# Kernel tuning notes

Hardware: AMD Instinct MI355X
Metric: run time of the kernel (lower is better)

## Reference

```python
import jax, jax.numpy as jnp
import numpy as np

N_NODES = 20000
N_EDGES = 240000
NUM_SPECIES = 4
NUM_BASIS = 16
MAX_RADIUS = 3.15
SQRT_NN = float(np.sqrt(12.0))  # num_neighbors normalization


def _cg121():
    # Clebsch-Gordan for 1e x 2e -> 1e in the real l=2 basis used below:
    # [xy, yz, (3z^2-1), zx, x^2-y^2] (component-normalized). Built from the
    # symmetric traceless matrix pairing M(a) @ v, normalized to unit Frobenius norm.
    s5, s15 = np.sqrt(5.0), np.sqrt(15.0)
    C = np.zeros((3, 5, 3))
    for A in range(5):
        a = np.zeros(5); a[A] = 1.0
        M = np.zeros((3, 3))
        M[0, 1] = M[1, 0] = a[0] * s15 / 2
        M[1, 2] = M[2, 1] = a[1] * s15 / 2
        M[0, 2] = M[2, 0] = a[3] * s15 / 2
        M[0, 0] = -a[2] * s5 / 2 + a[4] * s15 / 2
        M[1, 1] = -a[2] * s5 / 2 - a[4] * s15 / 2
        M[2, 2] = a[2] * s5
        C[:, A, :] = M
    C /= np.linalg.norm(C)
    return jnp.asarray(C, dtype=jnp.float32)

CG121 = _cg121()


def silu(v):
    return v * jax.nn.sigmoid(v)


def lin0(h, W):  # equivariant linear on scalars: [N,u] x [u,v]
    return h @ W / np.sqrt(W.shape[0])


def lin1(h, W):  # equivariant linear on vectors: [N,u,3] x [u,v]
    return jnp.einsum('nuk,uv->nvk', h, W) / np.sqrt(W.shape[0])


def radial_mlp(hb, W1, W2):  # FullyConnectedNet([16,64,nw], silu), normalized weights
    h = silu(hb @ W1 / np.sqrt(W1.shape[0]))
    return h @ W2 / np.sqrt(W2.shape[0])


def radial_basis(r):
    # soft_one_hot_linspace(..., basis='smooth_finite', cutoff=True) * sqrt(NUM_BASIS)
    values = np.linspace(0.0, MAX_RADIUS, NUM_BASIS + 2, dtype=np.float32)[1:-1]
    step = float(values[1] - values[0])
    d = (r[:, None] - values) / step
    def sus(t):
        safe = jnp.where(t > 0, t, 1.0)
        return jnp.where(t > 0, jnp.exp(-1.0 / safe), 0.0)
    y = 1.14136 * float(np.exp(2.0)) * sus(1.0 + d) * sus(1.0 - d)
    return y * np.sqrt(float(NUM_BASIS))


def sph_harm(edge_vec):
    # normalize=True, normalization='component' real spherical harmonics, l=0,1,2
    r = jnp.linalg.norm(edge_vec, axis=1)
    u = edge_vec / r[:, None]
    ux, uy, uz = u[:, 0], u[:, 1], u[:, 2]
    sh1 = np.sqrt(3.0) * u
    sh2 = jnp.stack([np.sqrt(15.0) * ux * uy,
                     np.sqrt(15.0) * uy * uz,
                     np.sqrt(5.0) / 2 * (3 * uz * uz - 1.0),
                     np.sqrt(15.0) * uz * ux,
                     np.sqrt(15.0) / 2 * (ux * ux - uy * uy)], axis=1)
    return r, sh1, sh2


def _forward(x, edge_index, edge_vec, emb,
             L1_lin1_0, L1_W1, L1_W2, L1_lin2_0, L1_lin2_1, L1_sc_0,
             L2_lin1_0, L2_lin1_1, L2_W1, L2_W2, L2_lin2_0, L2_lin2_1, L2_sc_0, L2_sc_1,
             LO_lin1_0, LO_lin1_1, LO_W1, LO_W2, LO_lin2_0, LO_sc_0):
    src, dst = edge_index[0], edge_index[1]
    N = x.shape[0]
    h0 = emb[x]                                   # [N,64] node embedding
    r, sh1, sh2 = sph_harm(edge_vec)
    hb = radial_basis(r)                          # [E,16]

    # ---- interaction 1: 64x0e -> (144x0e + 16x1e) -> gate -> 128x0e + 16x1e
    sc0 = lin0(h0, L1_sc_0)                       # self-connection [N,144]
    x0 = lin0(h0, L1_lin1_0)[src]                 # [E,64]
    w = radial_mlp(hb, L1_W1, L1_W2)              # [E,128] TP weights (uvu)
    m0 = x0 * w[:, :64]                           # 0e x 0e -> 0e
    m1 = (x0 * w[:, 64:128])[:, :, None] * sh1[:, None, :]  # 0e x 1e -> 1e
    a0 = jax.ops.segment_sum(m0, dst, num_segments=N) / SQRT_NN
    a1 = jax.ops.segment_sum(m1, dst, num_segments=N) / SQRT_NN
    g0 = lin0(a0, L1_lin2_0) + sc0                # [N,144]
    g1 = lin1(a1, L1_lin2_1)                      # [N,16,3]
    h0 = silu(g0[:, :128])                        # gated scalars
    h1 = jax.nn.sigmoid(g0[:, 128:])[:, :, None] * g1  # gate 16x1e

    # ---- interaction 2: 128x0e+16x1e -> (144x0e + 176x1e mid) -> gate
    sc0 = lin0(h0, L2_sc_0)                       # [N,144]
    sc1 = lin1(h1, L2_sc_1)                       # [N,16,3]
    x0 = lin0(h0, L2_lin1_0)[src]                 # [E,128]
    x1 = lin1(h1, L2_lin1_1)[src]                 # [E,16,3]
    w = radial_mlp(hb, L2_W1, L2_W2)              # [E,320]
    m0a = x0 * w[:, :128]                                            # 0x0->0
    m0b = jnp.einsum('euk,ek->eu', x1, sh1) / np.sqrt(3.0) * w[:, 272:288]  # 1x1->0
    m1a = (x0 * w[:, 128:256])[:, :, None] * sh1[:, None, :]         # 0x1->1
    m1b = x1 * w[:, 256:272][:, :, None]                             # 1x0->1
    m1c = jnp.cross(x1, sh1[:, None, :]) / np.sqrt(6.0) * w[:, 288:304][:, :, None]  # 1x1->1
    m1d = jnp.einsum('eui,eA,iAk->euk', x1, sh2, CG121) * w[:, 304:320][:, :, None]  # 1x2->1
    mid0 = jnp.concatenate([m0a, m0b], axis=1)    # [E,144]
    mid1 = jnp.concatenate([m1a, m1b, m1c, m1d], axis=1)  # [E,176,3]
    a0 = jax.ops.segment_sum(mid0, dst, num_segments=N) / SQRT_NN
    a1 = jax.ops.segment_sum(mid1, dst, num_segments=N) / SQRT_NN
    g0 = lin0(a0, L2_lin2_0) + sc0
    g1 = lin1(a1, L2_lin2_1) + sc1
    h0 = silu(g0[:, :128])
    h1 = jax.nn.sigmoid(g0[:, 128:])[:, :, None] * g1

    # ---- output interaction: -> 4x0e
    sc0 = lin0(h0, LO_sc_0)                       # [N,4]
    x0 = lin0(h0, LO_lin1_0)[src]
    x1 = lin1(h1, LO_lin1_1)[src]
    w = radial_mlp(hb, LO_W1, LO_W2)              # [E,144]
    m0a = x0 * w[:, :128]
    m0b = jnp.einsum('euk,ek->eu', x1, sh1) / np.sqrt(3.0) * w[:, 128:144]
    a0 = jax.ops.segment_sum(jnp.concatenate([m0a, m0b], axis=1), dst, num_segments=N) / SQRT_NN
    return lin0(a0, LO_lin2_0) + sc0              # [N,4]


def setup_inputs() -> dict:
    key = jax.random.key(0)
    ks = jax.random.split(key, 32)
    f = lambda i, shape: jax.random.normal(ks[i], shape, dtype=jnp.float32)
    return {
        'x': jax.random.randint(ks[0], (N_NODES,), 0, NUM_SPECIES),
        'edge_index': jax.random.randint(ks[1], (2, N_EDGES), 0, N_NODES),
        'edge_vec': jax.random.normal(ks[2], (N_EDGES, 3), dtype=jnp.float32),
        'emb': f(3, (NUM_SPECIES, 64)),
        'L1_lin1_0': f(4, (64, 64)),
        'L1_W1': f(5, (16, 64)), 'L1_W2': f(6, (64, 128)),
        'L1_lin2_0': f(7, (64, 144)), 'L1_lin2_1': f(8, (64, 16)),
        'L1_sc_0': f(9, (64, 144)),
        'L2_lin1_0': f(10, (128, 128)), 'L2_lin1_1': f(11, (16, 16)),
        'L2_W1': f(12, (16, 64)), 'L2_W2': f(13, (64, 320)),
        'L2_lin2_0': f(14, (144, 144)), 'L2_lin2_1': f(15, (176, 16)),
        'L2_sc_0': f(16, (128, 144)), 'L2_sc_1': f(17, (16, 16)),
        'LO_lin1_0': f(18, (128, 128)), 'LO_lin1_1': f(19, (16, 16)),
        'LO_W1': f(20, (16, 64)), 'LO_W2': f(21, (64, 144)),
        'LO_lin2_0': f(22, (144, 4)), 'LO_sc_0': f(23, (128, 4)),
    }


def reference(x, edge_index, edge_vec, emb,
              L1_lin1_0, L1_W1, L1_W2, L1_lin2_0, L1_lin2_1, L1_sc_0,
              L2_lin1_0, L2_lin1_1, L2_W1, L2_W2, L2_lin2_0, L2_lin2_1, L2_sc_0, L2_sc_1,
              LO_lin1_0, LO_lin1_1, LO_W1, LO_W2, LO_lin2_0, LO_sc_0):
    return _forward(x, edge_index, edge_vec, emb,
                    L1_lin1_0, L1_W1, L1_W2, L1_lin2_0, L1_lin2_1, L1_sc_0,
                    L2_lin1_0, L2_lin1_1, L2_W1, L2_W2, L2_lin2_0, L2_lin2_1, L2_sc_0, L2_sc_1,
                    LO_lin1_0, LO_lin1_1, LO_W1, LO_W2, LO_lin2_0, LO_sc_0)
```

## Files before the change

kernel.cpp:

```cpp
#include <hip/hip_runtime.h>
#include <math.h>

#define N_NODES 20000
#define N_EDGES 240000

typedef _Float16 half2_t __attribute__((ext_vector_type(2)));
typedef _Float16 f16x8   __attribute__((ext_vector_type(8)));
typedef float    f32x4v  __attribute__((ext_vector_type(4)));

__device__ __forceinline__ float siluf(float v){ return v * (1.0f/(1.0f+__expf(-v))); }
__device__ __forceinline__ float sigmf(float v){ return 1.0f/(1.0f+__expf(-v)); }

__global__ void k_count(const int* __restrict__ ei, int* __restrict__ cnt){
  int e = blockIdx.x*blockDim.x + threadIdx.x;
  if (e < N_EDGES) atomicAdd(&cnt[ei[N_EDGES + e]], 1);
}

__global__ void k_scan(const int* __restrict__ cnt, int* __restrict__ off, int* __restrict__ pos){
  __shared__ int part[1024];
  int t = threadIdx.x;
  int c[20]; int s = 0;
  #pragma unroll
  for (int j=0;j<20;j++){
    int idx = t*20 + j;
    int v = (idx < N_NODES) ? cnt[idx] : 0;
    c[j] = s; s += v;
  }
  part[t] = s;
  __syncthreads();
  for (int d=1; d<1024; d<<=1){
    int add = (t>=d) ? part[t-d] : 0;
    __syncthreads();
    part[t] += add;
    __syncthreads();
  }
  int excl = part[t] - s;
  #pragma unroll
  for (int j=0;j<20;j++){
    int idx = t*20 + j;
    if (idx < N_NODES){ off[idx] = excl + c[j]; pos[idx] = excl + c[j]; }
  }
  if (t == 1023) off[N_NODES] = part[1023];
}

__global__ void k_scatter(const int* __restrict__ ei, int* __restrict__ pos,
                          int* __restrict__ perm, int* __restrict__ srcs){
  int e = blockIdx.x*blockDim.x + threadIdx.x;
  if (e >= N_EDGES) return;
  int d = ei[N_EDGES + e];
  int p = atomicAdd(&pos[d], 1);
  perm[e] = p;
  srcs[p] = ei[e];
}

__global__ void k_geom(const float* __restrict__ ev, const int* __restrict__ perm,
                       float* __restrict__ eg){
  int e = blockIdx.x*blockDim.x + threadIdx.x;
  if (e >= N_EDGES) return;
  float x = ev[3*e+0], y = ev[3*e+1], z = ev[3*e+2];
  float r = sqrtf(x*x + y*y + z*z);
  float inv = 1.0f / fmaxf(r, 1e-12f);
  float ux = x*inv, uy = y*inv, uz = z*inv;
  float* o = eg + (size_t)perm[e]*24;
  o[0] = 1.7320508f*ux; o[1] = 1.7320508f*uy; o[2] = 1.7320508f*uz;
  o[3] = 3.8729833f*ux*uy;
  o[4] = 3.8729833f*uy*uz;
  o[5] = 1.1180340f*(3.0f*uz*uz - 1.0f);
  o[6] = 3.8729833f*uz*ux;
  o[7] = 1.9364917f*(ux*ux - uy*uy);
  const float invstep = 17.0f/3.15f;
  float t = r*invstep;
  #pragma unroll
  for (int i=0;i<16;i++){
    float d = t - (float)(i+1);
    float a = 1.0f + d, b = 1.0f - d;
    float v = 0.0f;
    if (a > 0.0f && b > 0.0f) v = 33.734292f*__expf(-1.0f/a - 1.0f/b);
    o[8+i] = v;
  }
}

__global__ void k_node_l1(const int* __restrict__ xs, const float* __restrict__ emb,
                          const float* __restrict__ Wlin, const float* __restrict__ Wsc,
                          float* __restrict__ X0, float* __restrict__ SC0){
  __shared__ float hs[4][64];
  int n0 = blockIdx.x*4;
  int t  = threadIdx.x;
  {
    int j = t>>6, k = t&63;
    hs[j][k] = emb[xs[n0+j]*64 + k];
  }
  __syncthreads();
  if (t < 64){
    float acc[4] = {};
    for (int k=0;k<64;k++){
      float wv = Wlin[k*64 + t];
      #pragma unroll
      for (int j=0;j<4;j++) acc[j] += hs[j][k]*wv;
    }
    #pragma unroll
    for (int j=0;j<4;j++) X0[(size_t)(n0+j)*64 + t] = acc[j]*0.125f;
  } else if (t < 208){
    int o = t - 64;
    float acc[4] = {};
    for (int k=0;k<64;k++){
      float wv = Wsc[k*144 + o];
      #pragma unroll
      for (int j=0;j<4;j++) acc[j] += hs[j][k]*wv;
    }
    #pragma unroll
    for (int j=0;j<4;j++) SC0[(size_t)(n0+j)*144 + o] = acc[j]*0.125f;
  }
}

__global__ __launch_bounds__(256) void k_hidden(
    const float* __restrict__ EG, const float* __restrict__ W1,
    _Float16* __restrict__ H){
  __shared__ float w1s[16*64];
  int tid = threadIdx.x;
  for (int i=tid;i<16*64;i+=256) w1s[i] = W1[i]*0.25f;
  __syncthreads();
  int lane = tid & 63, wib = tid >> 6;
  int gw = blockIdx.x*4 + wib, nw = gridDim.x*4;
  for (int e = gw; e < N_EDGES; e += nw){
    const float* g8 = EG + (size_t)e*24 + 8;
    float a0 = 0.0f, a1 = 0.0f;
    #pragma unroll
    for (int b=0;b<8;b++){
      a0 = fmaf(g8[b],   w1s[b*64 + lane],     a0);
      a1 = fmaf(g8[8+b], w1s[(8+b)*64 + lane], a1);
    }
    H[(size_t)e*64 + lane] = (_Float16)siluf(a0 + a1);
  }
}

template<int MODE>
__device__ __forceinline__ float colscale(int c){
  if constexpr (MODE == 1){
    if (c >= 272 && c < 288) return 0.57735027f;
    if (c >= 288 && c < 304) return 0.40824829f;
    return 1.0f;
  } else if constexpr (MODE == 2){
    return (c >= 128) ? 0.57735027f : 1.0f;
  }
  return 1.0f;
}

template<int NT, int MODE>
__global__ __launch_bounds__(256) void k_ww_mfma(
    int e0c, int e1c, const _Float16* __restrict__ H,
    const float* __restrict__ W2, _Float16* __restrict__ WW){
  constexpr int NCOL = NT*16;
  constexpr int NTW  = (NT + 3) / 4;
  int tid = threadIdx.x;
  int lane = tid & 63, wib = tid >> 6;
  int row = lane & 15, quad = lane >> 4;
  const float fold = 0.125f*0.28867513f;
  f16x8 B0[NTW], B1[NTW];
  #pragma unroll
  for (int t2=0; t2<NTW; t2++){
    int ct = wib*NTW + t2;
    int c  = ct*16 + row;
    bool valid = (ct < NT);
    float fs = valid ? fold*colscale<MODE>(c) : 0.0f;
    int ci = valid ? c : 0;
    #pragma unroll
    for (int j=0;j<8;j++){
      B0[t2][j] = (_Float16)(W2[(quad*8+j)*NCOL + ci]*fs);
      B1[t2][j] = (_Float16)(W2[(32+quad*8+j)*NCOL + ci]*fs);
    }
  }
  int ntiles = (e1c - e0c) >> 4;
  for (int t = blockIdx.x; t < ntiles; t += gridDim.x){
    int eb = e0c + t*16;
    const _Float16* hp = H + (size_t)(eb + row)*64 + quad*8;
    f16x8 A0 = *(const f16x8*)hp;
    f16x8 A1 = *(const f16x8*)(hp + 32);
    #pragma unroll
    for (int t2=0; t2<NTW; t2++){
      int ct = wib*NTW + t2;
      f32x4v d = __builtin_amdgcn_mfma_f32_16x16x32_f16(A0, B0[t2], (f32x4v){0.f,0.f,0.f,0.f}, 0,0,0);
      d = __builtin_amdgcn_mfma_f32_16x16x32_f16(A1, B1[t2], d, 0,0,0);
      if (ct < NT){
        int c0 = ct*16;
        #pragma unroll
        for (int j=0;j<4;j++){
          WW[(size_t)(eb - e0c + quad*4 + j)*NCOL + c0 + row] = (_Float16)d[j];
        }
      }
    }
  }
}

__global__ __launch_bounds__(256) void k_gather_l1(
    const int* __restrict__ off, const int* __restrict__ srcs, const float* __restrict__ eg,
    const _Float16* __restrict__ WW, const float* __restrict__ X0,
    float* __restrict__ A0, float* __restrict__ A1, int e0, int e1){
  int tid = threadIdx.x, lane = tid & 63;
  int gw = (blockIdx.x*256 + tid) >> 6;
  int nw = (gridDim.x*256) >> 6;
  for (int n = gw; n < N_NODES; n += nw){
    int ib = off[n], ie = off[n+1];
    if (ib < e0) ib = e0;
    if (ie > e1) ie = e1;
    if (ib >= ie) continue;
    float a0a = 0.0f, a1a[3] = {0,0,0};
    for (int i = ib; i < ie; i++){
      const float* g = eg + (size_t)i*24;
      const _Float16* w = WW + (size_t)(i - e0)*128;
      float w0  = (float)w[lane];
      float w1v = (float)w[64 + lane];
      float x0 = X0[(size_t)srcs[i]*64 + lane];
      float m0 = x0*w0, m1 = x0*w1v;
      a0a += m0;
      a1a[0] += m1*g[0]; a1a[1] += m1*g[1]; a1a[2] += m1*g[2];
    }
    A0[(size_t)n*64 + lane] += a0a;
    float* p = A1 + (size_t)n*192 + lane*3;
    p[0] += a1a[0]; p[1] += a1a[1]; p[2] += a1a[2];
  }
}

__global__ __launch_bounds__(256) void k_gather_l2(
    const int* __restrict__ off, const int* __restrict__ srcs, const float* __restrict__ eg,
    const _Float16* __restrict__ WW, const float* __restrict__ X0, const float* __restrict__ X1,
    float* __restrict__ A0, float* __restrict__ A1, int e0, int e1){
  int tid = threadIdx.x, lane = tid & 63;
  int grp = lane >> 4, v = lane & 15;
  int gw = (blockIdx.x*256 + tid) >> 6;
  int nw = (gridDim.x*256) >> 6;
  for (int n = gw; n < N_NODES; n += nw){
    int ib = off[n], ie = off[n+1];
    if (ib < e0) ib = e0;
    if (ie > e1) ie = e1;
    if (ib >= ie) continue;
    float a0a=0.f, a0b=0.f, a0c=0.f;
    float a1a[3]={0,0,0}, a1b[3]={0,0,0}, a1g[3]={0,0,0};
    for (int i = ib; i < ie; i++){
      const float* g = eg + (size_t)i*24;
      int src = srcs[i];
      const _Float16* w = WW + (size_t)(i - e0)*320;
      float w0  = (float)w[lane];
      float w1v = (float)w[ 64 + lane];
      float w2v = (float)w[128 + lane];
      float w3v = (float)w[192 + lane];
      float w4  = (float)w[256 + lane];
      const float* x0p = X0 + (size_t)src*128;
      float x0a = x0p[lane], x0b = x0p[64 + lane];
      float sx = g[0], sy = g[1], sz = g[2];
      a0a += x0a*w0;
      a0b += x0b*w1v;
      float ma = x0a*w2v, mb = x0b*w3v;
      a1a[0] += ma*sx; a1a[1] += ma*sy; a1a[2] += ma*sz;
      a1b[0] += mb*sx; a1b[1] += mb*sy; a1b[2] += mb*sz;
      const float* x1p = X1 + (size_t)src*48 + v*3;
      float xx = x1p[0], xy = x1p[1], xz = x1p[2];
      if (grp == 0){
        a1g[0] += w4*xx; a1g[1] += w4*xy; a1g[2] += w4*xz;
      } else if (grp == 1){
        a0c += w4*(xx*sx + xy*sy + xz*sz);
      } else if (grp == 2){
        a1g[0] += w4*(xy*sz - xz*sy);
        a1g[1] += w4*(xz*sx - xx*sz);
        a1g[2] += w4*(xx*sy - xy*sx);
      } else {
        float s20=g[3], s21=g[4], s22=g[5], s23=g[6], s24=g[7];
        const float c1c = 0.31622777f, c2c = 0.18257419f;
        a1g[0] += w4*(xx*(c1c*s24 - c2c*s22) + xy*(c1c*s20)            + xz*(c1c*s23));
        a1g[1] += w4*(xx*(c1c*s20)           + xy*(-c2c*s22 - c1c*s24) + xz*(c1c*s21));
        a1g[2] += w4*(xx*(c1c*s23)           + xy*(c1c*s21)            + xz*(2.0f*c2c*s22));
      }
    }
    float* a0 = A0 + (size_t)n*144;
    float* a1 = A1 + (size_t)n*528;
    a0[lane] += a0a;
    a0[64 + lane] += a0b;
    if (grp == 1) a0[128 + v] += a0c;
    float* p = a1 + lane*3;
    p[0] += a1a[0]; p[1] += a1a[1]; p[2] += a1a[2];
    p = a1 + (64 + lane)*3;
    p[0] += a1b[0]; p[1] += a1b[1]; p[2] += a1b[2];
    int gbase = (grp == 0) ? 128 : (grp == 2) ? 144 : (grp == 3) ? 160 : -1;
    if (gbase >= 0){
      p = a1 + (gbase + v)*3;
      p[0] += a1g[0]; p[1] += a1g[1]; p[2] += a1g[2];
    }
  }
}

__global__ __launch_bounds__(256) void k_gather_lo(
    const int* __restrict__ off, const int* __restrict__ srcs, const float* __restrict__ eg,
    const _Float16* __restrict__ WW, const float* __restrict__ X0, const float* __restrict__ X1,
    float* __restrict__ A0, int e0, int e1){
  int tid = threadIdx.x, lane = tid & 63, v = lane & 15;
  int gw = (blockIdx.x*256 + tid) >> 6;
  int nw = (gridDim.x*256) >> 6;
  for (int n = gw; n < N_NODES; n += nw){
    int ib = off[n], ie = off[n+1];
    if (ib < e0) ib = e0;
    if (ie > e1) ie = e1;
    if (ib >= ie) continue;
    float a0a = 0.f, a0b = 0.f, a0c = 0.f;
    for (int i = ib; i < ie; i++){
      const float* g = eg + (size_t)i*24;
      int src = srcs[i];
      const _Float16* w = WW + (size_t)(i - e0)*144;
      float w0  = (float)w[lane];
      float w1v = (float)w[64 + lane];
      float w2v = (float)w[128 + v];
      const float* x0p = X0 + (size_t)src*128;
      a0a += x0p[lane]*w0;
      a0b += x0p[64 + lane]*w1v;
      const float* x1p = X1 + (size_t)src*48 + v*3;
      float dot = x1p[0]*g[0] + x1p[1]*g[1] + x1p[2]*g[2];
      a0c += w2v*dot;
    }
    float* a0 = A0 + (size_t)n*144;
    a0[lane] += a0a;
    a0[64 + lane] += a0b;
    if (lane < 16) a0[128 + lane] += a0c;
  }
}

__global__ void k_upd_l1(const float* __restrict__ A0, const float* __restrict__ A1,
                         const float* __restrict__ SC0,
                         const float* __restrict__ W20, const float* __restrict__ W21,
                         float* __restrict__ H0, float* __restrict__ H1){
  __shared__ float sig[8][16];
  __shared__ float g1s[8][48];
  int n0 = blockIdx.x*8, t = threadIdx.x;
  if (t < 144){
    float acc[8] = {};
    for (int k=0;k<64;k++){
      float wv = W20[k*144 + t];
      #pragma unroll
      for (int j=0;j<8;j++) acc[j] += A0[(size_t)(n0+j)*64 + k]*wv;
    }
    #pragma unroll
    for (int j=0;j<8;j++){
      float gg = acc[j]*0.125f + SC0[(size_t)(n0+j)*144 + t];
      if (t < 128) H0[(size_t)(n0+j)*128 + t] = siluf(gg);
      else         sig[j][t-128] = sigmf(gg);
    }
  } else if (t < 192){
    int idx = t-144, v = idx/3, k = idx%3;
    float acc[8] = {};
    for (int u=0;u<64;u++){
      float wv = W21[u*16 + v];
      #pragma unroll
      for (int j=0;j<8;j++) acc[j] += A1[(size_t)(n0+j)*192 + u*3 + k]*wv;
    }
    #pragma unroll
    for (int j=0;j<8;j++) g1s[j][idx] = acc[j]*0.125f;
  }
  __syncthreads();
  if (t >= 144 && t < 192){
    int idx = t-144, v = idx/3;
    #pragma unroll
    for (int j=0;j<8;j++) H1[(size_t)(n0+j)*48 + idx] = sig[j][v]*g1s[j][idx];
  }
}

__global__ void k_lin_l2(const float* __restrict__ H0, const float* __restrict__ H1,
                         const float* __restrict__ Wsc0, const float* __restrict__ Wsc1,
                         const float* __restrict__ Wl0,  const float* __restrict__ Wl1,
                         float* __restrict__ SC0, float* __restrict__ SC1,
                         float* __restrict__ X0,  float* __restrict__ X1){
  int n0 = blockIdx.x*8, t = threadIdx.x;
  const float is128 = 0.08838835f;
  if (t < 144){
    float acc[8] = {};
    for (int k=0;k<128;k++){
      float wv = Wsc0[k*144 + t];
      #pragma unroll
      for (int j=0;j<8;j++) acc[j] += H0[(size_t)(n0+j)*128 + k]*wv;
    }
    #pragma unroll
    for (int j=0;j<8;j++) SC0[(size_t)(n0+j)*144 + t] = acc[j]*is128;
  } else if (t < 192){
    int idx = t-144, v = idx/3, k = idx%3;
    float acc[8] = {};
    for (int u=0;u<16;u++){
      float wv = Wsc1[u*16 + v];
      #pragma unroll
      for (int j=0;j<8;j++) acc[j] += H1[(size_t)(n0+j)*48 + u*3 + k]*wv;
    }
    #pragma unroll
    for (int j=0;j<8;j++) SC1[(size_t)(n0+j)*48 + idx] = acc[j]*0.25f;
  } else if (t < 320){
    int o = t-192;
    float acc[8] = {};
    for (int k=0;k<128;k++){
      float wv = Wl0[k*128 + o];
      #pragma unroll
      for (int j=0;j<8;j++) acc[j] += H0[(size_t)(n0+j)*128 + k]*wv;
    }
    #pragma unroll
    for (int j=0;j<8;j++) X0[(size_t)(n0+j)*128 + o] = acc[j]*is128;
  } else if (t < 368){
    int idx = t-320, v = idx/3, k = idx%3;
    float acc[8] = {};
    for (int u=0;u<16;u++){
      float wv = Wl1[u*16 + v];
      #pragma unroll
      for (int j=0;j<8;j++) acc[j] += H1[(size_t)(n0+j)*48 + u*3 + k]*wv;
    }
    #pragma unroll
    for (int j=0;j<8;j++) X1[(size_t)(n0+j)*48 + idx] = acc[j]*0.25f;
  }
}

__global__ void k_upd_l2(const float* __restrict__ A0, const float* __restrict__ A1,
                         const float* __restrict__ SC0, const float* __restrict__ SC1,
                         const float* __restrict__ W20, const float* __restrict__ W21,
                         float* __restrict__ H0, float* __restrict__ H1){
  __shared__ float sig[8][16];
  __shared__ float g1s[8][48];
  int n0 = blockIdx.x*8, t = threadIdx.x;
  if (t < 144){
    float acc[8] = {};
    for (int k=0;k<144;k++){
      float wv = W20[k*144 + t];
      #pragma unroll
      for (int j=0;j<8;j++) acc[j] += A0[(size_t)(n0+j)*144 + k]*wv;
    }
    #pragma unroll
    for (int j=0;j<8;j++){
      float gg = acc[j]*(1.0f/12.0f) + SC0[(size_t)(n0+j)*144 + t];
      if (t < 128) H0[(size_t)(n0+j)*128 + t] = siluf(gg);
      else         sig[j][t-128] = sigmf(gg);
    }
  } else if (t < 192){
    int idx = t-144, v = idx/3, k = idx%3;
    float acc[8] = {};
    for (int u=0;u<176;u++){
      float wv = W21[u*16 + v];
      #pragma unroll
      for (int j=0;j<8;j++) acc[j] += A1[(size_t)(n0+j)*528 + u*3 + k]*wv;
    }
    #pragma unroll
    for (int j=0;j<8;j++) g1s[j][idx] = acc[j]*0.075377836f + SC1[(size_t)(n0+j)*48 + idx];
  }
  __syncthreads();
  if (t >= 144 && t < 192){
    int idx = t-144, v = idx/3;
    #pragma unroll
    for (int j=0;j<8;j++) H1[(size_t)(n0+j)*48 + idx] = sig[j][v]*g1s[j][idx];
  }
}

__global__ void k_lin_lo(const float* __restrict__ H0, const float* __restrict__ H1,
                         const float* __restrict__ Wsc0,
                         const float* __restrict__ Wl0, const float* __restrict__ Wl1,
                         float* __restrict__ SCO, float* __restrict__ X0, float* __restrict__ X1){
  int n0 = blockIdx.x*8, t = threadIdx.x;
  const float is128 = 0.08838835f;
  if (t < 4){
    float acc[8] = {};
    for (int k=0;k<128;k++){
      float wv = Wsc0[k*4 + t];
      #pragma unroll
      for (int j=0;j<8;j++) acc[j] += H0[(size_t)(n0+j)*128 + k]*wv;
    }
    #pragma unroll
    for (int j=0;j<8;j++) SCO[(size_t)(n0+j)*4 + t] = acc[j]*is128;
  } else if (t < 132){
    int o = t-4;
    float acc[8] = {};
    for (int k=0;k<128;k++){
      float wv = Wl0[k*128 + o];
      #pragma unroll
      for (int j=0;j<8;j++) acc[j] += H0[(size_t)(n0+j)*128 + k]*wv;
    }
    #pragma unroll
    for (int j=0;j<8;j++) X0[(size_t)(n0+j)*128 + o] = acc[j]*is128;
  } else if (t < 180){
    int idx = t-132, v = idx/3, k = idx%3;
    float acc[8] = {};
    for (int u=0;u<16;u++){
      float wv = Wl1[u*16 + v];
      #pragma unroll
      for (int j=0;j<8;j++) acc[j] += H1[(size_t)(n0+j)*48 + u*3 + k]*wv;
    }
    #pragma unroll
    for (int j=0;j<8;j++) X1[(size_t)(n0+j)*48 + idx] = acc[j]*0.25f;
  }
}

__global__ void k_final(const float* __restrict__ A0, const float* __restrict__ SCO,
                        const float* __restrict__ W, float* __restrict__ out){
  int i = blockIdx.x*blockDim.x + threadIdx.x;
  if (i >= N_NODES*4) return;
  int n = i >> 2, c = i & 3;
  const float* a0 = A0 + (size_t)n*144;
  float acc = 0.0f;
  for (int k=0;k<144;k++) acc += a0[k]*W[k*4 + c];
  out[i] = acc*(1.0f/12.0f) + SCO[i];
}

extern "C" void kernel_launch(void* const* d_in, const int* in_sizes, int n_in,
                              void* d_out, int out_size, void* d_ws, size_t ws_size,
                              hipStream_t stream) {
  const int*   x   = (const int*)  d_in[0];
  const int*   ei  = (const int*)  d_in[1];
  const float* ev  = (const float*)d_in[2];
  const float* emb = (const float*)d_in[3];
  const float* L1_lin1_0 = (const float*)d_in[4];
  const float* L1_W1     = (const float*)d_in[5];
  const float* L1_W2     = (const float*)d_in[6];
  const float* L1_lin2_0 = (const float*)d_in[7];
  const float* L1_lin2_1 = (const float*)d_in[8];
  const float* L1_sc_0   = (const float*)d_in[9];
  const float* L2_lin1_0 = (const float*)d_in[10];
  const float* L2_lin1_1 = (const float*)d_in[11];
  const float* L2_W1     = (const float*)d_in[12];
  const float* L2_W2     = (const float*)d_in[13];
  const float* L2_lin2_0 = (const float*)d_in[14];
  const float* L2_lin2_1 = (const float*)d_in[15];
  const float* L2_sc_0   = (const float*)d_in[16];
  const float* L2_sc_1   = (const float*)d_in[17];
  const float* LO_lin1_0 = (const float*)d_in[18];
  const float* LO_lin1_1 = (const float*)d_in[19];
  const float* LO_W1     = (const float*)d_in[20];
  const float* LO_W2     = (const float*)d_in[21];
  const float* LO_lin2_0 = (const float*)d_in[22];
  const float* LO_sc_0   = (const float*)d_in[23];
  float* out = (float*)d_out;

  int* cnt  = (int*)d_ws;
  int* off  = cnt  + N_NODES;
  int* pos  = off  + N_NODES + 1;
  int* perm = pos  + N_NODES;
  int* srcs = perm + N_EDGES;
  float* EG  = (float*)(((char*)d_ws) + ((size_t)540004 * 4));
  float* X0  = EG  + (size_t)N_EDGES*24;
  float* X1  = X0  + (size_t)N_NODES*128;
  float* SC0 = X1  + (size_t)N_NODES*48;
  float* SC1 = SC0 + (size_t)N_NODES*144;
  float* A0  = SC1 + (size_t)N_NODES*48;
  float* A1  = A0  + (size_t)N_NODES*144;
  float* H0  = A1  + (size_t)N_NODES*528;
  float* H1  = H0  + (size_t)N_NODES*128;
  _Float16* HH = (_Float16*)(H1 + (size_t)N_NODES*48);
  _Float16* WW = HH + (size_t)N_EDGES*64;

  size_t used = (size_t)((char*)WW - (char*)d_ws);
  size_t avail = (ws_size > used) ? (ws_size - used) : 0;
  auto chunk_for = [&](int ncol)->int{
    size_t ce = avail / ((size_t)ncol * sizeof(_Float16));
    if (ce >= (size_t)N_EDGES) return N_EDGES;
    int c = (int)ce & ~15;
    return c < 4096 ? 4096 : c;
  };

  hipMemsetAsync(cnt, 0, N_NODES*sizeof(int), stream);
  k_count  <<<(N_EDGES+255)/256, 256, 0, stream>>>(ei, cnt);
  k_scan   <<<1, 1024, 0, stream>>>(cnt, off, pos);
  k_scatter<<<(N_EDGES+255)/256, 256, 0, stream>>>(ei, pos, perm, srcs);
  k_geom   <<<(N_EDGES+255)/256, 256, 0, stream>>>(ev, perm, EG);

  k_node_l1<<<N_NODES/4, 256, 0, stream>>>(x, emb, L1_lin1_0, L1_sc_0, X0, SC0);
  hipMemsetAsync(A0, 0, (size_t)N_NODES*64*4,  stream);
  hipMemsetAsync(A1, 0, (size_t)N_NODES*192*4, stream);
  k_hidden<<<2048, 256, 0, stream>>>(EG, L1_W1, HH);
  {
    int chunk = chunk_for(128);
    for (int e0 = 0; e0 < N_EDGES; e0 += chunk){
      int e1 = (e0 + chunk < N_EDGES) ? e0 + chunk : N_EDGES;
      k_ww_mfma<8,0><<<2048, 256, 0, stream>>>(e0, e1, HH, L1_W2, WW);
      k_gather_l1<<<2500, 256, 0, stream>>>(off, srcs, EG, WW, X0, A0, A1, e0, e1);
    }
  }
  k_upd_l1<<<N_NODES/8, 256, 0, stream>>>(A0, A1, SC0, L1_lin2_0, L1_lin2_1, H0, H1);

  k_lin_l2<<<N_NODES/8, 384, 0, stream>>>(H0, H1, L2_sc_0, L2_sc_1, L2_lin1_0, L2_lin1_1,
                                          SC0, SC1, X0, X1);
  hipMemsetAsync(A0, 0, (size_t)N_NODES*144*4, stream);
  hipMemsetAsync(A1, 0, (size_t)N_NODES*528*4, stream);
  k_hidden<<<2048, 256, 0, stream>>>(EG, L2_W1, HH);
  {
    int chunk = chunk_for(320);
    for (int e0 = 0; e0 < N_EDGES; e0 += chunk){
      int e1 = (e0 + chunk < N_EDGES) ? e0 + chunk : N_EDGES;
      k_ww_mfma<20,1><<<2048, 256, 0, stream>>>(e0, e1, HH, L2_W2, WW);
      k_gather_l2<<<2500, 256, 0, stream>>>(off, srcs, EG, WW, X0, X1, A0, A1, e0, e1);
    }
  }
  k_upd_l2<<<N_NODES/8, 256, 0, stream>>>(A0, A1, SC0, SC1, L2_lin2_0, L2_lin2_1, H0, H1);

  k_lin_lo<<<N_NODES/8, 256, 0, stream>>>(H0, H1, LO_sc_0, LO_lin1_0, LO_lin1_1, SC1, X0, X1);
  hipMemsetAsync(A0, 0, (size_t)N_NODES*144*4, stream);
  k_hidden<<<2048, 256, 0, stream>>>(EG, LO_W1, HH);
  {
    int chunk = chunk_for(144);
    for (int e0 = 0; e0 < N_EDGES; e0 += chunk){
      int e1 = (e0 + chunk < N_EDGES) ? e0 + chunk : N_EDGES;
      k_ww_mfma<9,2><<<2048, 256, 0, stream>>>(e0, e1, HH, LO_W2, WW);
      k_gather_lo<<<2500, 256, 0, stream>>>(off, srcs, EG, WW, X0, X1, A0, e0, e1);
    }
  }
  k_final<<<(N_NODES*4+255)/256, 256, 0, stream>>>(A0, SC1, LO_lin2_0, out);
}
```

Before: 753.5 us.

## Drop accumulator memsets, stage node rows in LDS for update/linear kernels

The gather kernels gain a `first` flag so the first edge chunk writes the accumulators directly instead of adding into zeroed buffers, which removes five memset passes over large node arrays. The per-node update, linear and final kernels now copy their eight input node rows into shared memory with vectorized float4 loads before the matmul loops, replacing repeated strided global reads. k_final is restructured to process eight nodes per block. The cost is extra LDS use and a sync in each block, and the last kernel leaves most threads idle.

```diff
diff --git a/kernel.cpp b/kernel.cpp
--- a/kernel.cpp
+++ b/kernel.cpp
@@ -195,7 +195,7 @@
 __global__ __launch_bounds__(256) void k_gather_l1(
     const int* __restrict__ off, const int* __restrict__ srcs, const float* __restrict__ eg,
     const _Float16* __restrict__ WW, const float* __restrict__ X0,
-    float* __restrict__ A0, float* __restrict__ A1, int e0, int e1){
+    float* __restrict__ A0, float* __restrict__ A1, int e0, int e1, int first){
   int tid = threadIdx.x, lane = tid & 63;
   int gw = (blockIdx.x*256 + tid) >> 6;
   int nw = (gridDim.x*256) >> 6;
@@ -203,7 +203,7 @@
     int ib = off[n], ie = off[n+1];
     if (ib < e0) ib = e0;
     if (ie > e1) ie = e1;
-    if (ib >= ie) continue;
+    if (!first && ib >= ie) continue;
     float a0a = 0.0f, a1a[3] = {0,0,0};
     for (int i = ib; i < ie; i++){
       const float* g = eg + (size_t)i*24;
@@ -215,16 +215,21 @@
       a0a += m0;
       a1a[0] += m1*g[0]; a1a[1] += m1*g[1]; a1a[2] += m1*g[2];
     }
-    A0[(size_t)n*64 + lane] += a0a;
     float* p = A1 + (size_t)n*192 + lane*3;
-    p[0] += a1a[0]; p[1] += a1a[1]; p[2] += a1a[2];
+    if (first){
+      A0[(size_t)n*64 + lane] = a0a;
+      p[0] = a1a[0]; p[1] = a1a[1]; p[2] = a1a[2];
+    } else {
+      A0[(size_t)n*64 + lane] += a0a;
+      p[0] += a1a[0]; p[1] += a1a[1]; p[2] += a1a[2];
+    }
   }
 }
 
 __global__ __launch_bounds__(256) void k_gather_l2(
     const int* __restrict__ off, const int* __restrict__ srcs, const float* __restrict__ eg,
     const _Float16* __restrict__ WW, const float* __restrict__ X0, const float* __restrict__ X1,
-    float* __restrict__ A0, float* __restrict__ A1, int e0, int e1){
+    float* __restrict__ A0, float* __restrict__ A1, int e0, int e1, int first){
   int tid = threadIdx.x, lane = tid & 63;
   int grp = lane >> 4, v = lane & 15;
   int gw = (blockIdx.x*256 + tid) >> 6;
@@ -233,7 +238,7 @@
     int ib = off[n], ie = off[n+1];
     if (ib < e0) ib = e0;
     if (ie > e1) ie = e1;
-    if (ib >= ie) continue;
+    if (!first && ib >= ie) continue;
     float a0a=0.f, a0b=0.f, a0c=0.f;
     float a1a[3]={0,0,0}, a1b[3]={0,0,0}, a1g[3]={0,0,0};
     for (int i = ib; i < ie; i++){
@@ -273,17 +278,31 @@
     }
     float* a0 = A0 + (size_t)n*144;
     float* a1 = A1 + (size_t)n*528;
-    a0[lane] += a0a;
-    a0[64 + lane] += a0b;
-    if (grp == 1) a0[128 + v] += a0c;
-    float* p = a1 + lane*3;
-    p[0] += a1a[0]; p[1] += a1a[1]; p[2] += a1a[2];
-    p = a1 + (64 + lane)*3;
-    p[0] += a1b[0]; p[1] += a1b[1]; p[2] += a1b[2];
     int gbase = (grp == 0) ? 128 : (grp == 2) ? 144 : (grp == 3) ? 160 : -1;
-    if (gbase >= 0){
-      p = a1 + (gbase + v)*3;
-      p[0] += a1g[0]; p[1] += a1g[1]; p[2] += a1g[2];
+    if (first){
+      a0[lane] = a0a;
+      a0[64 + lane] = a0b;
+      if (grp == 1) a0[128 + v] = a0c;
+      float* p = a1 + lane*3;
+      p[0] = a1a[0]; p[1] = a1a[1]; p[2] = a1a[2];
+      p = a1 + (64 + lane)*3;
+      p[0] = a1b[0]; p[1] = a1b[1]; p[2] = a1b[2];
+      if (gbase >= 0){
+        p = a1 + (gbase + v)*3;
+        p[0] = a1g[0]; p[1] = a1g[1]; p[2] = a1g[2];
+      }
+    } else {
+      a0[lane] += a0a;
+      a0[64 + lane] += a0b;
+      if (grp == 1) a0[128 + v] += a0c;
+      float* p = a1 + lane*3;
+      p[0] += a1a[0]; p[1] += a1a[1]; p[2] += a1a[2];
+      p = a1 + (64 + lane)*3;
+      p[0] += a1b[0]; p[1] += a1b[1]; p[2] += a1b[2];
+      if (gbase >= 0){
+        p = a1 + (gbase + v)*3;
+        p[0] += a1g[0]; p[1] += a1g[1]; p[2] += a1g[2];
+      }
     }
   }
 }
@@ -291,7 +310,7 @@
 __global__ __launch_bounds__(256) void k_gather_lo(
     const int* __restrict__ off, const int* __restrict__ srcs, const float* __restrict__ eg,
     const _Float16* __restrict__ WW, const float* __restrict__ X0, const float* __restrict__ X1,
-    float* __restrict__ A0, int e0, int e1){
+    float* __restrict__ A0, int e0, int e1, int first){
   int tid = threadIdx.x, lane = tid & 63, v = lane & 15;
   int gw = (blockIdx.x*256 + tid) >> 6;
   int nw = (gridDim.x*256) >> 6;
@@ -299,7 +318,7 @@
     int ib = off[n], ie = off[n+1];
     if (ib < e0) ib = e0;
     if (ie > e1) ie = e1;
-    if (ib >= ie) continue;
+    if (!first && ib >= ie) continue;
     float a0a = 0.f, a0b = 0.f, a0c = 0.f;
     for (int i = ib; i < ie; i++){
       const float* g = eg + (size_t)i*24;
@@ -316,25 +335,43 @@
       a0c += w2v*dot;
     }
     float* a0 = A0 + (size_t)n*144;
-    a0[lane] += a0a;
-    a0[64 + lane] += a0b;
-    if (lane < 16) a0[128 + lane] += a0c;
-  }
-}
-
-__global__ void k_upd_l1(const float* __restrict__ A0, const float* __restrict__ A1,
-                         const float* __restrict__ SC0,
-                         const float* __restrict__ W20, const float* __restrict__ W21,
-                         float* __restrict__ H0, float* __restrict__ H1){
+    if (first){
+      a0[lane] = a0a;
+      a0[64 + lane] = a0b;
+      if (lane < 16) a0[128 + lane] = a0c;
+    } else {
+      a0[lane] += a0a;
+      a0[64 + lane] += a0b;
+      if (lane < 16) a0[128 + lane] += a0c;
+    }
+  }
+}
+
+__global__ __launch_bounds__(256) void k_upd_l1(
+    const float* __restrict__ A0, const float* __restrict__ A1,
+    const float* __restrict__ SC0,
+    const float* __restrict__ W20, const float* __restrict__ W21,
+    float* __restrict__ H0, float* __restrict__ H1){
+  __shared__ float a0s[8*64];
+  __shared__ float a1s[8*192];
   __shared__ float sig[8][16];
   __shared__ float g1s[8][48];
   int n0 = blockIdx.x*8, t = threadIdx.x;
+  {
+    const float4* s0 = (const float4*)(A0 + (size_t)n0*64);
+    float4* d0 = (float4*)a0s;
+    for (int i=t;i<8*64/4;i+=256) d0[i] = s0[i];
+    const float4* s1 = (const float4*)(A1 + (size_t)n0*192);
+    float4* d1 = (float4*)a1s;
+    for (int i=t;i<8*192/4;i+=256) d1[i] = s1[i];
+  }
+  __syncthreads();
   if (t < 144){
     float acc[8] = {};
     for (int k=0;k<64;k++){
       float wv = W20[k*144 + t];
       #pragma unroll
-      for (int j=0;j<8;j++) acc[j] += A0[(size_t)(n0+j)*64 + k]*wv;
+      for (int j=0;j<8;j++) acc[j] += a0s[j*64 + k]*wv;
     }
     #pragma unroll
     for (int j=0;j<8;j++){
@@ -348,7 +385,7 @@
     for (int u=0;u<64;u++){
       float wv = W21[u*16 + v];
       #pragma unroll
-      for (int j=0;j<8;j++) acc[j] += A1[(size_t)(n0+j)*192 + u*3 + k]*wv;
+      for (int j=0;j<8;j++) acc[j] += a1s[j*192 + u*3 + k]*wv;
     }
     #pragma unroll
     for (int j=0;j<8;j++) g1s[j][idx] = acc[j]*0.125f;
@@ -361,19 +398,31 @@
   }
 }
 
-__global__ void k_lin_l2(const float* __restrict__ H0, const float* __restrict__ H1,
-                         const float* __restrict__ Wsc0, const float* __restrict__ Wsc1,
-                         const float* __restrict__ Wl0,  const float* __restrict__ Wl1,
-                         float* __restrict__ SC0, float* __restrict__ SC1,
-                         float* __restrict__ X0,  float* __restrict__ X1){
+__global__ __launch_bounds__(384) void k_lin_l2(
+    const float* __restrict__ H0, const float* __restrict__ H1,
+    const float* __restrict__ Wsc0, const float* __restrict__ Wsc1,
+    const float* __restrict__ Wl0,  const float* __restrict__ Wl1,
+    float* __restrict__ SC0, float* __restrict__ SC1,
+    float* __restrict__ X0,  float* __restrict__ X1){
+  __shared__ float h0s[8*128];
+  __shared__ float h1s[8*48];
   int n0 = blockIdx.x*8, t = threadIdx.x;
+  {
+    const float4* s0 = (const float4*)(H0 + (size_t)n0*128);
+    float4* d0 = (float4*)h0s;
+    for (int i=t;i<8*128/4;i+=384) d0[i] = s0[i];
+    const float4* s1 = (const float4*)(H1 + (size_t)n0*48);
+    float4* d1 = (float4*)h1s;
+    for (int i=t;i<8*48/4;i+=384) d1[i] = s1[i];
+  }
+  __syncthreads();
   const float is128 = 0.08838835f;
   if (t < 144){
     float acc[8] = {};
     for (int k=0;k<128;k++){
       float wv = Wsc0[k*144 + t];
       #pragma unroll
-      for (int j=0;j<8;j++) acc[j] += H0[(size_t)(n0+j)*128 + k]*wv;
+      for (int j=0;j<8;j++) acc[j] += h0s[j*128 + k]*wv;
     }
     #pragma unroll
     for (int j=0;j<8;j++) SC0[(size_t)(n0+j)*144 + t] = acc[j]*is128;
@@ -383,7 +432,7 @@
     for (int u=0;u<16;u++){
       float wv = Wsc1[u*16 + v];
       #pragma unroll
-      for (int j=0;j<8;j++) acc[j] += H1[(size_t)(n0+j)*48 + u*3 + k]*wv;
+      for (int j=0;j<8;j++) acc[j] += h1s[j*48 + u*3 + k]*wv;
     }
     #pragma unroll
     for (int j=0;j<8;j++) SC1[(size_t)(n0+j)*48 + idx] = acc[j]*0.25f;
@@ -393,7 +442,7 @@
     for (int k=0;k<128;k++){
       float wv = Wl0[k*128 + o];
       #pragma unroll
-      for (int j=0;j<8;j++) acc[j] += H0[(size_t)(n0+j)*128 + k]*wv;
+      for (int j=0;j<8;j++) acc[j] += h0s[j*128 + k]*wv;
     }
     #pragma unroll
     for (int j=0;j<8;j++) X0[(size_t)(n0+j)*128 + o] = acc[j]*is128;
@@ -403,26 +452,38 @@
     for (int u=0;u<16;u++){
       float wv = Wl1[u*16 + v];
       #pragma unroll
-      for (int j=0;j<8;j++) acc[j] += H1[(size_t)(n0+j)*48 + u*3 + k]*wv;
+      for (int j=0;j<8;j++) acc[j] += h1s[j*48 + u*3 + k]*wv;
     }
     #pragma unroll
     for (int j=0;j<8;j++) X1[(size_t)(n0+j)*48 + idx] = acc[j]*0.25f;
   }
 }
 
-__global__ void k_upd_l2(const float* __restrict__ A0, const float* __restrict__ A1,
-                         const float* __restrict__ SC0, const float* __restrict__ SC1,
-                         const float* __restrict__ W20, const float* __restrict__ W21,
-                         float* __restrict__ H0, float* __restrict__ H1){
+__global__ __launch_bounds__(256) void k_upd_l2(
+    const float* __restrict__ A0, const float* __restrict__ A1,
+    const float* __restrict__ SC0, const float* __restrict__ SC1,
+    const float* __restrict__ W20, const float* __restrict__ W21,
+    float* __restrict__ H0, float* __restrict__ H1){
+  __shared__ float a0s[8*144];
+  __shared__ float a1s[8*528];
   __shared__ float sig[8][16];
   __shared__ float g1s[8][48];
   int n0 = blockIdx.x*8, t = threadIdx.x;
+  {
+    const float4* s0 = (const float4*)(A0 + (size_t)n0*144);
+    float4* d0 = (float4*)a0s;
+    for (int i=t;i<8*144/4;i+=256) d0[i] = s0[i];
+    const float4* s1 = (const float4*)(A1 + (size_t)n0*528);
+    float4* d1 = (float4*)a1s;
+    for (int i=t;i<8*528/4;i+=256) d1[i] = s1[i];
+  }
+  __syncthreads();
   if (t < 144){
     float acc[8] = {};
     for (int k=0;k<144;k++){
       float wv = W20[k*144 + t];
       #pragma unroll
-      for (int j=0;j<8;j++) acc[j] += A0[(size_t)(n0+j)*144 + k]*wv;
+      for (int j=0;j<8;j++) acc[j] += a0s[j*144 + k]*wv;
     }
     #pragma unroll
     for (int j=0;j<8;j++){
@@ -436,7 +497,7 @@
     for (int u=0;u<176;u++){
       float wv = W21[u*16 + v];
       #pragma unroll
-      for (int j=0;j<8;j++) acc[j] += A1[(size_t)(n0+j)*528 + u*3 + k]*wv;
+      for (int j=0;j<8;j++) acc[j] += a1s[j*528 + u*3 + k]*wv;
     }
     #pragma unroll
     for (int j=0;j<8;j++) g1s[j][idx] = acc[j]*0.075377836f + SC1[(size_t)(n0+j)*48 + idx];
@@ -449,18 +510,30 @@
   }
 }
 
-__global__ void k_lin_lo(const float* __restrict__ H0, const float* __restrict__ H1,
-                         const float* __restrict__ Wsc0,
-                         const float* __restrict__ Wl0, const float* __restrict__ Wl1,
-                         float* __restrict__ SCO, float* __restrict__ X0, float* __restrict__ X1){
+__global__ __launch_bounds__(256) void k_lin_lo(
+    const float* __restrict__ H0, const float* __restrict__ H1,
+    const float* __restrict__ Wsc0,
+    const float* __restrict__ Wl0, const float* __restrict__ Wl1,
+    float* __restrict__ SCO, float* __restrict__ X0, float* __restrict__ X1){
+  __shared__ float h0s[8*128];
+  __shared__ float h1s[8*48];
   int n0 = blockIdx.x*8, t = threadIdx.x;
+  {
+    const float4* s0 = (const float4*)(H0 + (size_t)n0*128);
+    float4* d0 = (float4*)h0s;
+    for (int i=t;i<8*128/4;i+=256) d0[i] = s0[i];
+    const float4* s1 = (const float4*)(H1 + (size_t)n0*48);
+    float4* d1 = (float4*)h1s;
+    for (int i=t;i<8*48/4;i+=256) d1[i] = s1[i];
+  }
+  __syncthreads();
   const float is128 = 0.08838835f;
   if (t < 4){
     float acc[8] = {};
     for (int k=0;k<128;k++){
       float wv = Wsc0[k*4 + t];
       #pragma unroll
-      for (int j=0;j<8;j++) acc[j] += H0[(size_t)(n0+j)*128 + k]*wv;
+      for (int j=0;j<8;j++) acc[j] += h0s[j*128 + k]*wv;
     }
     #pragma unroll
     for (int j=0;j<8;j++) SCO[(size_t)(n0+j)*4 + t] = acc[j]*is128;
@@ -470,7 +543,7 @@
     for (int k=0;k<128;k++){
       float wv = Wl0[k*128 + o];
       #pragma unroll
-      for (int j=0;j<8;j++) acc[j] += H0[(size_t)(n0+j)*128 + k]*wv;
+      for (int j=0;j<8;j++) acc[j] += h0s[j*128 + k]*wv;
     }
     #pragma unroll
     for (int j=0;j<8;j++) X0[(size_t)(n0+j)*128 + o] = acc[j]*is128;
@@ -480,22 +553,31 @@
     for (int u=0;u<16;u++){
       float wv = Wl1[u*16 + v];
       #pragma unroll
-      for (int j=0;j<8;j++) acc[j] += H1[(size_t)(n0+j)*48 + u*3 + k]*wv;
+      for (int j=0;j<8;j++) acc[j] += h1s[j*48 + u*3 + k]*wv;
     }
     #pragma unroll
     for (int j=0;j<8;j++) X1[(size_t)(n0+j)*48 + idx] = acc[j]*0.25f;
   }
 }
 
-__global__ void k_final(const float* __restrict__ A0, const float* __restrict__ SCO,
-                        const float* __restrict__ W, float* __restrict__ out){
-  int i = blockIdx.x*blockDim.x + threadIdx.x;
-  if (i >= N_NODES*4) return;
-  int n = i >> 2, c = i & 3;
-  const float* a0 = A0 + (size_t)n*144;
-  float acc = 0.0f;
-  for (int k=0;k<144;k++) acc += a0[k]*W[k*4 + c];
-  out[i] = acc*(1.0f/12.0f) + SCO[i];
+__global__ __launch_bounds__(256) void k_final(
+    const float* __restrict__ A0, const float* __restrict__ SCO,
+    const float* __restrict__ W, float* __restrict__ out){
+  __shared__ float a0s[8*144];
+  int n0 = blockIdx.x*8, t = threadIdx.x;
+  {
+    const float4* s0 = (const float4*)(A0 + (size_t)n0*144);
+    float4* d0 = (float4*)a0s;
+    for (int i=t;i<8*144/4;i+=256) d0[i] = s0[i];
+  }
+  __syncthreads();
+  if (t < 32){
+    int j = t >> 2, c = t & 3;
+    float acc = 0.0f;
+    for (int k=0;k<144;k++) acc += a0s[j*144 + k]*W[k*4 + c];
+    int i = (n0 + j)*4 + c;
+    out[i] = acc*(1.0f/12.0f) + SCO[i];
+  }
 }
 
 extern "C" void kernel_launch(void* const* d_in, const int* in_sizes, int n_in,
@@ -560,44 +642,39 @@
   k_geom   <<<(N_EDGES+255)/256, 256, 0, stream>>>(ev, perm, EG);
 
   k_node_l1<<<N_NODES/4, 256, 0, stream>>>(x, emb, L1_lin1_0, L1_sc_0, X0, SC0);
-  hipMemsetAsync(A0, 0, (size_t)N_NODES*64*4,  stream);
-  hipMemsetAsync(A1, 0, (size_t)N_NODES*192*4, stream);
   k_hidden<<<2048, 256, 0, stream>>>(EG, L1_W1, HH);
   {
     int chunk = chunk_for(128);
     for (int e0 = 0; e0 < N_EDGES; e0 += chunk){
       int e1 = (e0 + chunk < N_EDGES) ? e0 + chunk : N_EDGES;
       k_ww_mfma<8,0><<<2048, 256, 0, stream>>>(e0, e1, HH, L1_W2, WW);
-      k_gather_l1<<<2500, 256, 0, stream>>>(off, srcs, EG, WW, X0, A0, A1, e0, e1);
+      k_gather_l1<<<2500, 256, 0, stream>>>(off, srcs, EG, WW, X0, A0, A1, e0, e1, e0==0);
     }
   }
   k_upd_l1<<<N_NODES/8, 256, 0, stream>>>(A0, A1, SC0, L1_lin2_0, L1_lin2_1, H0, H1);
 
   k_lin_l2<<<N_NODES/8, 384, 0, stream>>>(H0, H1, L2_sc_0, L2_sc_1, L2_lin1_0, L2_lin1_1,
                                           SC0, SC1, X0, X1);
-  hipMemsetAsync(A0, 0, (size_t)N_NODES*144*4, stream);
-  hipMemsetAsync(A1, 0, (size_t)N_NODES*528*4, stream);
   k_hidden<<<2048, 256, 0, stream>>>(EG, L2_W1, HH);
   {
     int chunk = chunk_for(320);
     for (int e0 = 0; e0 < N_EDGES; e0 += chunk){
       int e1 = (e0 + chunk < N_EDGES) ? e0 + chunk : N_EDGES;
       k_ww_mfma<20,1><<<2048, 256, 0, stream>>>(e0, e1, HH, L2_W2, WW);
-      k_gather_l2<<<2500, 256, 0, stream>>>(off, srcs, EG, WW, X0, X1, A0, A1, e0, e1);
+      k_gather_l2<<<2500, 256, 0, stream>>>(off, srcs, EG, WW, X0, X1, A0, A1, e0, e1, e0==0);
     }
   }
   k_upd_l2<<<N_NODES/8, 256, 0, stream>>>(A0, A1, SC0, SC1, L2_lin2_0, L2_lin2_1, H0, H1);
 
   k_lin_lo<<<N_NODES/8, 256, 0, stream>>>(H0, H1, LO_sc_0, LO_lin1_0, LO_lin1_1, SC1, X0, X1);
-  hipMemsetAsync(A0, 0, (size_t)N_NODES*144*4, stream);
   k_hidden<<<2048, 256, 0, stream>>>(EG, LO_W1, HH);
   {
     int chunk = chunk_for(144);
     for (int e0 = 0; e0 < N_EDGES; e0 += chunk){
       int e1 = (e0 + chunk < N_EDGES) ? e0 + chunk : N_EDGES;
       k_ww_mfma<9,2><<<2048, 256, 0, stream>>>(e0, e1, HH, LO_W2, WW);
-      k_gather_lo<<<2500, 256, 0, stream>>>(off, srcs, EG, WW, X0, X1, A0, e0, e1);
-    }
-  }
-  k_final<<<(N_NODES*4+255)/256, 256, 0, stream>>>(A0, SC1, LO_lin2_0, out);
-}
+      k_gather_lo<<<2500, 256, 0, stream>>>(off, srcs, EG, WW, X0, X1, A0, e0, e1, e0==0);
+    }
+  }
+  k_final<<<N_NODES/8, 256, 0, stream>>>(A0, SC1, LO_lin2_0, out);
+}
```

Result: faster. 701.7 us (-6.9%).
